# Kernel optimization log

Measured on AMD Instinct MI355X. Metric: run time of the kernel, lower is better.

## Reference

```python
import jax, jax.numpy as jnp
import numpy as np

B, T, C, H = 2, 2048, 1024, 16
D = C // H  # head dim 64

def setup_inputs() -> dict:
    key = jax.random.key(0)
    k1, k2, k3 = jax.random.split(key, 3)
    x = jax.random.normal(k1, (B, T, C), dtype=jnp.float32)
    W_attn = jax.random.normal(k2, (C, 3 * C), dtype=jnp.float32) * (1.0 / np.sqrt(C))
    b_attn = jnp.zeros((3 * C,), dtype=jnp.float32)
    W_proj = jax.random.normal(k3, (C, C), dtype=jnp.float32) * (1.0 / np.sqrt(C))
    b_proj = jnp.zeros((C,), dtype=jnp.float32)
    return {"x": x, "W_attn": W_attn, "b_attn": b_attn, "W_proj": W_proj, "b_proj": b_proj}

def reference(x, W_attn, b_attn, W_proj, b_proj):
    Bsz, Tlen, Cdim = x.shape
    qkv = x @ W_attn + b_attn  # [B,T,3C]
    q, k, v = jnp.split(qkv, 3, axis=2)
    # [B,T,C] -> [B,H,T,D]
    q = q.reshape(Bsz, Tlen, H, D).transpose(0, 2, 1, 3)
    k = k.reshape(Bsz, Tlen, H, D).transpose(0, 2, 1, 3)
    v = v.reshape(Bsz, Tlen, H, D).transpose(0, 2, 1, 3)
    att = jnp.einsum('bhqd,bhkd->bhqk', q, k) * (1.0 / np.sqrt(D))
    causal = jnp.tril(jnp.ones((Tlen, Tlen), dtype=bool))
    att = jnp.where(causal[None, None, :, :], att, jnp.float32(-jnp.inf))
    att = jax.nn.softmax(att, axis=-1)
    y = jnp.einsum('bhqk,bhkd->bhqd', att, v)  # [B,H,T,D]
    y = y.transpose(0, 2, 1, 3).reshape(Bsz, Tlen, Cdim)
    return y @ W_proj + b_proj
```

## Files before the change

kernel.cpp:

```cpp
#include <hip/hip_runtime.h>
#include <math.h>

#define BSZ 2
#define TSEQ 2048
#define CDIM 1024
#define HNUM 16

typedef __attribute__((ext_vector_type(8))) short bhalf8;
typedef __attribute__((ext_vector_type(4))) short bhalf4;
typedef __attribute__((ext_vector_type(4))) float floatx4;

__device__ __forceinline__ unsigned short f2bf(float f) {
    union { float f; unsigned u; } v;
    v.f = f;
    unsigned r = v.u + 0x7FFFu + ((v.u >> 16) & 1u);
    return (unsigned short)(r >> 16);
}

__device__ __forceinline__ floatx4 fx4_zero() { floatx4 z = {0.f,0.f,0.f,0.f}; return z; }

typedef __attribute__((address_space(3))) unsigned int lds_u32;
typedef const __attribute__((address_space(1))) unsigned int g_u32;
__device__ __forceinline__ void async_copy16(const void* g, void* l) {
    __builtin_amdgcn_global_load_lds((g_u32*)g, (lds_u32*)l, 16, 0, 0);
}

__global__ __launch_bounds__(256) void conv_bf16(
    const float* __restrict__ x, unsigned short* __restrict__ xb)
{
    size_t i = ((size_t)blockIdx.x * 256 + threadIdx.x) * 8;
    float4 a = *(const float4*)(x + i);
    float4 b = *(const float4*)(x + i + 4);
    uint4 o;
    o.x = (unsigned)f2bf(a.x) | ((unsigned)f2bf(a.y) << 16);
    o.y = (unsigned)f2bf(a.z) | ((unsigned)f2bf(a.w) << 16);
    o.z = (unsigned)f2bf(b.x) | ((unsigned)f2bf(b.y) << 16);
    o.w = (unsigned)f2bf(b.z) | ((unsigned)f2bf(b.w) << 16);
    *(uint4*)(xb + i) = o;
}

__global__ __launch_bounds__(256) void transpose_bf16(
    const float* __restrict__ W, unsigned short* __restrict__ Wt, int K, int N)
{
    __shared__ float t[32][33];
    const int n0 = blockIdx.x * 32, k0 = blockIdx.y * 32;
    const int tx = threadIdx.x & 31, ty = threadIdx.x >> 5;
#pragma unroll
    for (int i = 0; i < 4; ++i)
        t[ty + i * 8][tx] = W[(size_t)(k0 + ty + i * 8) * N + n0 + tx];
    __syncthreads();
#pragma unroll
    for (int i = 0; i < 4; ++i)
        Wt[(size_t)(n0 + ty + i * 8) * K + k0 + tx] = f2bf(t[tx][ty + i * 8]);
}

__global__ __launch_bounds__(256) void vtrans(
    const unsigned short* __restrict__ qkv, unsigned short* __restrict__ vT)
{
    __shared__ unsigned short tt[64][80];
    const int b  = blockIdx.z;
    const int ty = blockIdx.y * 64;
    const int cx = blockIdx.x * 64;
    const int tid = threadIdx.x;
    const int lr = tid >> 2, lc = (tid & 3) * 16;

    const unsigned short* src =
        qkv + (size_t)(b * 2048 + ty + lr) * 3072 + 2048 + cx + lc;
    uint4 v0 = *(const uint4*)src;
    uint4 v1 = *(const uint4*)(src + 8);
    tt[lc + 0][lr]  = (unsigned short)(v0.x & 0xffff);
    tt[lc + 1][lr]  = (unsigned short)(v0.x >> 16);
    tt[lc + 2][lr]  = (unsigned short)(v0.y & 0xffff);
    tt[lc + 3][lr]  = (unsigned short)(v0.y >> 16);
    tt[lc + 4][lr]  = (unsigned short)(v0.z & 0xffff);
    tt[lc + 5][lr]  = (unsigned short)(v0.z >> 16);
    tt[lc + 6][lr]  = (unsigned short)(v0.w & 0xffff);
    tt[lc + 7][lr]  = (unsigned short)(v0.w >> 16);
    tt[lc + 8][lr]  = (unsigned short)(v1.x & 0xffff);
    tt[lc + 9][lr]  = (unsigned short)(v1.x >> 16);
    tt[lc + 10][lr] = (unsigned short)(v1.y & 0xffff);
    tt[lc + 11][lr] = (unsigned short)(v1.y >> 16);
    tt[lc + 12][lr] = (unsigned short)(v1.z & 0xffff);
    tt[lc + 13][lr] = (unsigned short)(v1.z >> 16);
    tt[lc + 14][lr] = (unsigned short)(v1.w & 0xffff);
    tt[lc + 15][lr] = (unsigned short)(v1.w >> 16);
    __syncthreads();
    unsigned short* dst = vT + (size_t)(b * 1024 + cx + lr) * 2048 + ty + lc;
    *(uint4*)dst       = *(const uint4*)&tt[lr][lc];
    *(uint4*)(dst + 8) = *(const uint4*)&tt[lr][lc + 8];
}

template<int BM, bool OUT_BF16>
__global__ __launch_bounds__(256) void gemm_bt(
    const unsigned short* __restrict__ A, const unsigned short* __restrict__ Bt,
    const float* __restrict__ bias, void* __restrict__ Cp,
    int M, int N, int K)
{
    constexpr int ALINES = BM / 64;
    constexpr int MT = BM / 32;
    __shared__ unsigned short As[2][BM * 32];
    __shared__ unsigned short Bs[2][128 * 32];

    const int tid   = threadIdx.x;
    const int bm    = blockIdx.y;
    const int bn    = blockIdx.x;
    const int wave  = tid >> 6;
    const int col16 = tid & 15;
    const int quad  = (tid & 63) >> 4;
    const int wm    = (wave >> 1) * (BM / 2);
    const int wn    = (wave & 1) * 64;

    floatx4 acc[MT][4];
#pragma unroll
    for (int i = 0; i < MT; ++i)
#pragma unroll
        for (int j = 0; j < 4; ++j) acc[i][j] = fx4_zero();

    const int gr = tid >> 2;
    const int gk = (tid & 3) * 8;
    const unsigned short* Ab = A  + (size_t)(bm * BM + gr) * K + gk;
    const unsigned short* Bb = Bt + (size_t)(bn * 128 + gr) * K + gk;

#define STAGE(k0, bf) { \
    char* AsB = (char*)As[bf] + wave * 1024; \
    char* BsB = (char*)Bs[bf] + wave * 1024; \
    _Pragma("unroll") \
    for (int l = 0; l < ALINES; ++l) \
        async_copy16(Ab + (size_t)l * 64 * K + (k0), AsB + l * 4096); \
    async_copy16(Bb + (k0), BsB); \
    async_copy16(Bb + (size_t)64 * K + (k0), BsB + 4096); }

#define COMPUTE(bf) { \
    bhalf8 a[MT], b[4]; \
    _Pragma("unroll") \
    for (int i = 0; i < MT; ++i) \
        a[i] = *(const bhalf8*)&As[bf][(wm + i * 16 + col16) * 32 + quad * 8]; \
    _Pragma("unroll") \
    for (int j = 0; j < 4; ++j) \
        b[j] = *(const bhalf8*)&Bs[bf][(wn + j * 16 + col16) * 32 + quad * 8]; \
    _Pragma("unroll") \
    for (int i = 0; i < MT; ++i) \
        _Pragma("unroll") \
        for (int j = 0; j < 4; ++j) \
            acc[i][j] = __builtin_amdgcn_mfma_f32_16x16x32_bf16(a[i], b[j], acc[i][j], 0, 0, 0); }

    STAGE(0, 0);
    __syncthreads();
    int buf = 0;
    for (int k0 = 0; k0 < K - 32; k0 += 32) {
        STAGE(k0 + 32, buf ^ 1);
        COMPUTE(buf);
        __syncthreads();
        buf ^= 1;
    }
    COMPUTE(buf);
#undef STAGE
#undef COMPUTE

#pragma unroll
    for (int j = 0; j < 4; ++j) {
        int col = bn * 128 + wn + j * 16 + col16;
        float bv = bias[col];
#pragma unroll
        for (int i = 0; i < MT; ++i) {
#pragma unroll
            for (int r = 0; r < 4; ++r) {
                int row = bm * BM + wm + i * 16 + quad * 4 + r;
                float v = acc[i][j][r] + bv;
                if (OUT_BF16)
                    ((unsigned short*)Cp)[(size_t)row * N + col] = f2bf(v);
                else
                    ((float*)Cp)[(size_t)row * N + col] = v;
            }
        }
    }
}

template<bool DIAG>
__device__ __forceinline__ void attn_tile(
    const unsigned short* __restrict__ Ks, const unsigned short* __restrict__ Vt,
    const bhalf8* qf, floatx4* oT, float& l_part,
    int col16, int quad, int qloc)
{
    const float C_MUL = 0.125f * 1.44269504f;
    const float C_SUB = 17.31234049f;
    const int sx = col16 & 7;

    floatx4 s[4];
#pragma unroll
    for (int n = 0; n < 4; ++n) {
        const int row = 16 * n + col16;
        bhalf8 k0 = *(const bhalf8*)&Ks[row * 64 + ((quad ^ sx) * 8)];
        bhalf8 k1 = *(const bhalf8*)&Ks[row * 64 + (((4 + quad) ^ sx) * 8)];
        floatx4 t = __builtin_amdgcn_mfma_f32_16x16x32_bf16(k0, qf[0], fx4_zero(), 0, 0, 0);
        s[n] = __builtin_amdgcn_mfma_f32_16x16x32_bf16(k1, qf[1], t, 0, 0, 0);
    }

    bhalf4 pb[4];
#pragma unroll
    for (int n = 0; n < 4; ++n) {
        unsigned a[4];
#pragma unroll
        for (int r = 0; r < 4; ++r) {
            float p = exp2f(fmaf(s[n][r], C_MUL, -C_SUB));
            if (DIAG) {
                if (16 * n + quad * 4 + r > qloc) p = 0.f;
            }
            l_part += p;
            a[r] = __float_as_uint(p) + 0x8000u;
        }
        union { unsigned u[2]; bhalf4 b; } uu;
        uu.u[0] = (a[0] >> 16) | (a[1] & 0xffff0000u);
        uu.u[1] = (a[2] >> 16) | (a[3] & 0xffff0000u);
        pb[n] = uu.b;
    }

#pragma unroll
    for (int n = 0; n < 4; ++n) {
#pragma unroll
        for (int dt = 0; dt < 4; ++dt) {
            const int d = 16 * dt + col16;
            const bhalf4 av = *(const bhalf4*)
                &Vt[n * 1024 + ((d + n) & 63) * 16 + (quad >> 1) * 8 + (quad & 1) * 4];
            oT[dt] = __builtin_amdgcn_mfma_f32_16x16x16bf16_1k(av, pb[n], oT[dt], 0, 0, 0);
        }
    }
}

__global__ __launch_bounds__(256) void attn_mfma(
    const unsigned short* __restrict__ qkv,
    const unsigned short* __restrict__ vT,
    unsigned short* __restrict__ yout)
{
    __shared__ unsigned short Kbuf[2][64 * 64];
    __shared__ unsigned short Vbuf[2][64 * 64];

    const int tid   = threadIdx.x;
    const int wave  = tid >> 6;
    const int col16 = tid & 15;
    const int quad  = (tid & 63) >> 4;
    const int qb    = (int)gridDim.y - 1 - (int)blockIdx.y;
    const int bh    = blockIdx.x;
    const int b     = bh >> 4;
    const int h     = bh & 15;

    const unsigned short* base  = qkv + (size_t)b * TSEQ * 3072 + h * 64;
    const unsigned short* kbase = base + CDIM;
    const unsigned short* vtb   = vT + (size_t)(b * 1024 + h * 64) * 2048;

    bhalf8 qf[2];
    {
        const unsigned short* qrow =
            base + (size_t)(qb * 64 + wave * 16 + col16) * 3072 + quad * 8;
        qf[0] = *(const bhalf8*)qrow;
        qf[1] = *(const bhalf8*)(qrow + 32);
    }

    const int krow = tid >> 3;
    const int kchk = (tid & 7) ^ (krow & 7);
    const unsigned short* ksrc0 = kbase + (size_t)krow * 3072 + kchk * 8;
    const unsigned short* ksrc1 = kbase + (size_t)(krow + 32) * 3072 + kchk * 8;

    int L0 = tid, L1 = tid + 256;
    const int d0 = (((L0 >> 1) & 63) - ((L0 >> 1) >> 6)) & 63;
    const int c0 = 2 * ((L0 >> 1) >> 6) + (L0 & 1);
    const int d1 = (((L1 >> 1) & 63) - ((L1 >> 1) >> 6)) & 63;
    const int c1 = 2 * ((L1 >> 1) >> 6) + (L1 & 1);
    const unsigned short* vsrc0 = vtb + (size_t)d0 * 2048 + c0 * 8;
    const unsigned short* vsrc1 = vtb + (size_t)d1 * 2048 + c1 * 8;

#define ASTAGE(kb, bf) { \
    char* Kd = (char*)Kbuf[bf] + wave * 1024; \
    char* Vd = (char*)Vbuf[bf] + wave * 1024; \
    async_copy16(ksrc0 + (size_t)(kb) * 64 * 3072, Kd); \
    async_copy16(ksrc1 + (size_t)(kb) * 64 * 3072, Kd + 4096); \
    async_copy16(vsrc0 + (kb) * 64, Vd); \
    async_copy16(vsrc1 + (kb) * 64, Vd + 4096); }

    floatx4 oT[4];
#pragma unroll
    for (int dt = 0; dt < 4; ++dt) oT[dt] = fx4_zero();
    float l_part = 0.f;
    const int qloc = wave * 16 + col16;

    ASTAGE(0, 0);
    __syncthreads();
    int buf = 0;
    for (int kb = 0; kb < qb; ++kb) {
        ASTAGE(kb + 1, buf ^ 1);
        attn_tile<false>(Kbuf[buf], Vbuf[buf], qf, oT, l_part, col16, quad, qloc);
        __syncthreads();
        buf ^= 1;
    }
    attn_tile<true>(Kbuf[buf], Vbuf[buf], qf, oT, l_part, col16, quad, qloc);
#undef ASTAGE

    float l = l_part;
    l += __shfl_xor(l, 16);
    l += __shfl_xor(l, 32);
    const float inv = 1.0f / l;
    const size_t row = (size_t)b * TSEQ + (size_t)qb * 64 + wave * 16 + col16;
#pragma unroll
    for (int dt = 0; dt < 4; ++dt) {
        ushort4 o;
        o.x = f2bf(oT[dt][0] * inv);
        o.y = f2bf(oT[dt][1] * inv);
        o.z = f2bf(oT[dt][2] * inv);
        o.w = f2bf(oT[dt][3] * inv);
        *(ushort4*)(yout + row * CDIM + h * 64 + 16 * dt + quad * 4) = o;
    }
}

extern "C" void kernel_launch(void* const* d_in, const int* in_sizes, int n_in,
                              void* d_out, int out_size, void* d_ws, size_t ws_size,
                              hipStream_t stream)
{
    const float* x      = (const float*)d_in[0];
    const float* W_attn = (const float*)d_in[1];
    const float* b_attn = (const float*)d_in[2];
    const float* W_proj = (const float*)d_in[3];
    const float* b_proj = (const float*)d_in[4];
    float* out = (float*)d_out;

    unsigned short* qkv = (unsigned short*)d_ws;
    unsigned short* y   = qkv + (size_t)4096 * 3072;
    unsigned short* xb  = y   + (size_t)4096 * 1024;
    unsigned short* WtA = xb  + (size_t)4096 * 1024;
    unsigned short* WtP = WtA + (size_t)3072 * 1024;
    unsigned short* vT  = WtP + (size_t)1024 * 1024;

    conv_bf16<<<dim3((4096 * 1024) / (256 * 8)), 256, 0, stream>>>(x, xb);
    transpose_bf16<<<dim3(3072 / 32, 1024 / 32), 256, 0, stream>>>(W_attn, WtA, 1024, 3072);
    transpose_bf16<<<dim3(1024 / 32, 1024 / 32), 256, 0, stream>>>(W_proj, WtP, 1024, 1024);

    gemm_bt<128, true><<<dim3(3072 / 128, 4096 / 128), 256, 0, stream>>>(
        xb, WtA, b_attn, qkv, 4096, 3072, 1024);
    vtrans<<<dim3(16, 32, 2), 256, 0, stream>>>(qkv, vT);
    attn_mfma<<<dim3(BSZ * HNUM, TSEQ / 64), 256, 0, stream>>>(qkv, vT, y);
    gemm_bt<64, false><<<dim3(1024 / 128, 4096 / 64), 256, 0, stream>>>(
        y, WtP, b_proj, out, 4096, 1024, 1024);
}
```

Measured before the change: 198.1 us.

## Fuse V transpose into QKV GEMM epilogue and use padded V tiles in attention

The QKV GEMM epilogue now writes the V columns directly in transposed [b, d, t] layout with 4-wide vector stores, so the separate vtrans kernel and its extra pass over V are gone. In the attention kernel, V tiles are loaded through registers into a padded LDS layout with a row stride of 76, replacing the swizzled async global-to-LDS copies. This removes one launch and a round trip through memory. The cost is a register-staged V load, which may overlap less well with compute than the async copy did.

```diff
diff --git a/kernel.cpp b/kernel.cpp
--- a/kernel.cpp
+++ b/kernel.cpp
@@ -54,47 +54,11 @@
         Wt[(size_t)(n0 + ty + i * 8) * K + k0 + tx] = f2bf(t[tx][ty + i * 8]);
 }
 
-__global__ __launch_bounds__(256) void vtrans(
-    const unsigned short* __restrict__ qkv, unsigned short* __restrict__ vT)
-{
-    __shared__ unsigned short tt[64][80];
-    const int b  = blockIdx.z;
-    const int ty = blockIdx.y * 64;
-    const int cx = blockIdx.x * 64;
-    const int tid = threadIdx.x;
-    const int lr = tid >> 2, lc = (tid & 3) * 16;
-
-    const unsigned short* src =
-        qkv + (size_t)(b * 2048 + ty + lr) * 3072 + 2048 + cx + lc;
-    uint4 v0 = *(const uint4*)src;
-    uint4 v1 = *(const uint4*)(src + 8);
-    tt[lc + 0][lr]  = (unsigned short)(v0.x & 0xffff);
-    tt[lc + 1][lr]  = (unsigned short)(v0.x >> 16);
-    tt[lc + 2][lr]  = (unsigned short)(v0.y & 0xffff);
-    tt[lc + 3][lr]  = (unsigned short)(v0.y >> 16);
-    tt[lc + 4][lr]  = (unsigned short)(v0.z & 0xffff);
-    tt[lc + 5][lr]  = (unsigned short)(v0.z >> 16);
-    tt[lc + 6][lr]  = (unsigned short)(v0.w & 0xffff);
-    tt[lc + 7][lr]  = (unsigned short)(v0.w >> 16);
-    tt[lc + 8][lr]  = (unsigned short)(v1.x & 0xffff);
-    tt[lc + 9][lr]  = (unsigned short)(v1.x >> 16);
-    tt[lc + 10][lr] = (unsigned short)(v1.y & 0xffff);
-    tt[lc + 11][lr] = (unsigned short)(v1.y >> 16);
-    tt[lc + 12][lr] = (unsigned short)(v1.z & 0xffff);
-    tt[lc + 13][lr] = (unsigned short)(v1.z >> 16);
-    tt[lc + 14][lr] = (unsigned short)(v1.w & 0xffff);
-    tt[lc + 15][lr] = (unsigned short)(v1.w >> 16);
-    __syncthreads();
-    unsigned short* dst = vT + (size_t)(b * 1024 + cx + lr) * 2048 + ty + lc;
-    *(uint4*)dst       = *(const uint4*)&tt[lr][lc];
-    *(uint4*)(dst + 8) = *(const uint4*)&tt[lr][lc + 8];
-}
-
 template<int BM, bool OUT_BF16>
 __global__ __launch_bounds__(256) void gemm_bt(
     const unsigned short* __restrict__ A, const unsigned short* __restrict__ Bt,
     const float* __restrict__ bias, void* __restrict__ Cp,
-    int M, int N, int K)
+    int M, int N, int K, int v_start, unsigned short* __restrict__ vt)
 {
     constexpr int ALINES = BM / 64;
     constexpr int MT = BM / 32;
@@ -157,20 +121,33 @@
 #undef STAGE
 #undef COMPUTE
 
+    const int colbase = bn * 128 + wn;
+    const bool vpath = (v_start >= 0) && (colbase >= v_start);
 #pragma unroll
     for (int j = 0; j < 4; ++j) {
-        int col = bn * 128 + wn + j * 16 + col16;
+        int col = colbase + j * 16 + col16;
         float bv = bias[col];
 #pragma unroll
         for (int i = 0; i < MT; ++i) {
-#pragma unroll
-            for (int r = 0; r < 4; ++r) {
-                int row = bm * BM + wm + i * 16 + quad * 4 + r;
-                float v = acc[i][j][r] + bv;
-                if (OUT_BF16)
-                    ((unsigned short*)Cp)[(size_t)row * N + col] = f2bf(v);
-                else
-                    ((float*)Cp)[(size_t)row * N + col] = v;
+            if (vpath) {
+                int row0 = bm * BM + wm + i * 16 + quad * 4;
+                ushort4 o;
+                o.x = f2bf(acc[i][j][0] + bv);
+                o.y = f2bf(acc[i][j][1] + bv);
+                o.z = f2bf(acc[i][j][2] + bv);
+                o.w = f2bf(acc[i][j][3] + bv);
+                size_t vrow = (size_t)((row0 >> 11) * 1024 + (col - v_start));
+                *(ushort4*)(vt + vrow * 2048 + (row0 & 2047)) = o;
+            } else {
+#pragma unroll
+                for (int r = 0; r < 4; ++r) {
+                    int row = bm * BM + wm + i * 16 + quad * 4 + r;
+                    float v = acc[i][j][r] + bv;
+                    if (OUT_BF16)
+                        ((unsigned short*)Cp)[(size_t)row * N + col] = f2bf(v);
+                    else
+                        ((float*)Cp)[(size_t)row * N + col] = v;
+                }
             }
         }
     }
@@ -220,8 +197,7 @@
 #pragma unroll
         for (int dt = 0; dt < 4; ++dt) {
             const int d = 16 * dt + col16;
-            const bhalf4 av = *(const bhalf4*)
-                &Vt[n * 1024 + ((d + n) & 63) * 16 + (quad >> 1) * 8 + (quad & 1) * 4];
+            const bhalf4 av = *(const bhalf4*)&Vt[d * 76 + 16 * n + quad * 4];
             oT[dt] = __builtin_amdgcn_mfma_f32_16x16x16bf16_1k(av, pb[n], oT[dt], 0, 0, 0);
         }
     }
@@ -233,7 +209,7 @@
     unsigned short* __restrict__ yout)
 {
     __shared__ unsigned short Kbuf[2][64 * 64];
-    __shared__ unsigned short Vbuf[2][64 * 64];
+    __shared__ unsigned short Vbuf[2][64 * 76];
 
     const int tid   = threadIdx.x;
     const int wave  = tid >> 6;
@@ -261,21 +237,15 @@
     const unsigned short* ksrc0 = kbase + (size_t)krow * 3072 + kchk * 8;
     const unsigned short* ksrc1 = kbase + (size_t)(krow + 32) * 3072 + kchk * 8;
 
-    int L0 = tid, L1 = tid + 256;
-    const int d0 = (((L0 >> 1) & 63) - ((L0 >> 1) >> 6)) & 63;
-    const int c0 = 2 * ((L0 >> 1) >> 6) + (L0 & 1);
-    const int d1 = (((L1 >> 1) & 63) - ((L1 >> 1) >> 6)) & 63;
-    const int c1 = 2 * ((L1 >> 1) >> 6) + (L1 & 1);
-    const unsigned short* vsrc0 = vtb + (size_t)d0 * 2048 + c0 * 8;
-    const unsigned short* vsrc1 = vtb + (size_t)d1 * 2048 + c1 * 8;
-
-#define ASTAGE(kb, bf) { \
+    const int vd  = tid >> 3;
+    const int vt0 = (tid & 7) * 8;
+    const unsigned short* vsrc0 = vtb + (size_t)vd * 2048 + vt0;
+    const unsigned short* vsrc1 = vtb + (size_t)(vd + 32) * 2048 + vt0;
+
+#define KSTAGE(kb, bf) { \
     char* Kd = (char*)Kbuf[bf] + wave * 1024; \
-    char* Vd = (char*)Vbuf[bf] + wave * 1024; \
     async_copy16(ksrc0 + (size_t)(kb) * 64 * 3072, Kd); \
-    async_copy16(ksrc1 + (size_t)(kb) * 64 * 3072, Kd + 4096); \
-    async_copy16(vsrc0 + (kb) * 64, Vd); \
-    async_copy16(vsrc1 + (kb) * 64, Vd + 4096); }
+    async_copy16(ksrc1 + (size_t)(kb) * 64 * 3072, Kd + 4096); }
 
     floatx4 oT[4];
 #pragma unroll
@@ -283,17 +253,27 @@
     float l_part = 0.f;
     const int qloc = wave * 16 + col16;
 
-    ASTAGE(0, 0);
+    {
+        uint4 nv0 = *(const uint4*)vsrc0;
+        uint4 nv1 = *(const uint4*)vsrc1;
+        KSTAGE(0, 0);
+        *(uint4*)&Vbuf[0][vd * 76 + vt0]        = nv0;
+        *(uint4*)&Vbuf[0][(vd + 32) * 76 + vt0] = nv1;
+    }
     __syncthreads();
     int buf = 0;
     for (int kb = 0; kb < qb; ++kb) {
-        ASTAGE(kb + 1, buf ^ 1);
+        uint4 nv0 = *(const uint4*)(vsrc0 + (size_t)(kb + 1) * 64);
+        uint4 nv1 = *(const uint4*)(vsrc1 + (size_t)(kb + 1) * 64);
+        KSTAGE(kb + 1, buf ^ 1);
         attn_tile<false>(Kbuf[buf], Vbuf[buf], qf, oT, l_part, col16, quad, qloc);
+        *(uint4*)&Vbuf[buf ^ 1][vd * 76 + vt0]        = nv0;
+        *(uint4*)&Vbuf[buf ^ 1][(vd + 32) * 76 + vt0] = nv1;
         __syncthreads();
         buf ^= 1;
     }
     attn_tile<true>(Kbuf[buf], Vbuf[buf], qf, oT, l_part, col16, quad, qloc);
-#undef ASTAGE
+#undef KSTAGE
 
     float l = l_part;
     l += __shfl_xor(l, 16);
@@ -334,9 +314,8 @@
     transpose_bf16<<<dim3(1024 / 32, 1024 / 32), 256, 0, stream>>>(W_proj, WtP, 1024, 1024);
 
     gemm_bt<128, true><<<dim3(3072 / 128, 4096 / 128), 256, 0, stream>>>(
-        xb, WtA, b_attn, qkv, 4096, 3072, 1024);
-    vtrans<<<dim3(16, 32, 2), 256, 0, stream>>>(qkv, vT);
+        xb, WtA, b_attn, qkv, 4096, 3072, 1024, 2048, vT);
     attn_mfma<<<dim3(BSZ * HNUM, TSEQ / 64), 256, 0, stream>>>(qkv, vT, y);
     gemm_bt<64, false><<<dim3(1024 / 128, 4096 / 64), 256, 0, stream>>>(
-        y, WtP, b_proj, out, 4096, 1024, 1024);
-}
+        y, WtP, b_proj, out, 4096, 1024, 1024, -1, nullptr);
+}
```

Result: faster. 188.4 us (-4.9%).
